# Performance work log

Hardware: AMD Instinct MI355X
Metric: run time of the kernel (lower is better)

Reference implementation:

```python
import jax, jax.numpy as jnp
import numpy as np

EPS = 1e-4


def setup_inputs() -> dict:
    key = jax.random.key(0)
    k1, k2, k3 = jax.random.split(key, 3)
    B, C, H, W = 8, 3, 1024, 1024
    n_axis, n_knots = 8, 16
    raw = jax.random.uniform(k1, (B, C, H, W), dtype=jnp.float32)
    ys = jax.random.uniform(k2, (B, n_axis, n_knots), dtype=jnp.float32)
    A = jax.random.normal(k3, (B, C, n_axis), dtype=jnp.float32)
    return {"raw": raw, "ys": ys, "A": A}


def reference(raw, ys, A):
    # raw: [B,3,H,W], ys: [B,n_axis,K], A: [B,3,n_axis]
    B, C, H, W = raw.shape
    K = ys.shape[-1]
    pinv_A = jnp.linalg.pinv(A)                      # [B, n_axis, 3]
    mins = jnp.sum(A * (A < 0), axis=1)              # [B, n_axis]
    maxs = jnp.sum(A * (A > 0), axis=1)              # [B, n_axis]

    # project pixels onto axes: [B, n_axis, H, W]
    f = jnp.einsum('bchw,bca->bahw', raw, A)

    # knot x-positions (uniform per batch/axis): [B, n_axis, K+2]
    t = jnp.linspace(0.0, 1.0, K + 2, dtype=raw.dtype)[None, None]
    xs = t * (maxs + EPS - mins)[..., None] + mins[..., None]
    ys_full = jnp.concatenate([mins[..., None], ys, maxs[..., None]], axis=-1)  # [B,A,K+2]
    dx = xs[..., 1] - xs[..., 0]                     # [B, n_axis]
    slopes = jnp.diff(ys_full, axis=-1) / dx[..., None]  # [B, n_axis, K+1]

    # segment index per pixel (replaces masked loop): floor((f - xs0)/dx)
    idx = jnp.clip(jnp.floor((f - mins[..., None, None]) / dx[..., None, None]),
                   0, K).astype(jnp.int32)           # [B, n_axis, H, W]

    idx_flat = idx.reshape(B, -1, H * W)             # [B, n_axis, HW]
    ys_hi = jnp.take_along_axis(ys_full, idx_flat + 1, axis=-1).reshape(f.shape)
    xs_hi = jnp.take_along_axis(xs, idx_flat + 1, axis=-1).reshape(f.shape)
    sl = jnp.take_along_axis(slopes, idx_flat, axis=-1).reshape(f.shape)

    est = ys_hi - (xs_hi - f) * sl                   # [B, n_axis, H, W]

    # project back to RGB: [B, 3, H, W]
    out = jnp.einsum('bahw,bac->bchw', est, pinv_A)
    return out
```

## Files before the change

kernel.cpp:

```cpp
#include <hip/hip_runtime.h>

#define EPS 1e-4f
#define NAXIS 8
#define NKNOTS 16
#define NSEG 17
#define WS_STRIDE 384

typedef float fv4 __attribute__((ext_vector_type(4)));

__global__ void spline_prep(const float* __restrict__ ys,
                            const float* __restrict__ A,
                            float* __restrict__ ws) {
    const int b = blockIdx.x;
    const float* Ab  = A  + (size_t)b * 3 * NAXIS;
    const float* ysb = ys + (size_t)b * NAXIS * NKNOTS;
    float* w = ws + (size_t)b * WS_STRIDE;
    __shared__ double Ginv[9];
    const int tid = threadIdx.x;

    if (tid == 0) {
        double G[9];
        for (int i = 0; i < 3; ++i)
            for (int j = 0; j < 3; ++j) {
                double s = 0.0;
                for (int a = 0; a < NAXIS; ++a)
                    s += (double)Ab[i * NAXIS + a] * (double)Ab[j * NAXIS + a];
                G[i * 3 + j] = s;
            }
        const double g00 = G[0], g01 = G[1], g02 = G[2];
        const double g11 = G[4], g12 = G[5], g22 = G[8];
        const double det = g00 * (g11 * g22 - g12 * g12)
                         - g01 * (g01 * g22 - g12 * g02)
                         + g02 * (g01 * g12 - g11 * g02);
        const double inv = 1.0 / det;
        Ginv[0] = (g11 * g22 - g12 * g12) * inv;
        Ginv[1] = (g02 * g12 - g01 * g22) * inv;
        Ginv[2] = (g01 * g12 - g02 * g11) * inv;
        Ginv[3] = Ginv[1];
        Ginv[4] = (g00 * g22 - g02 * g02) * inv;
        Ginv[5] = (g02 * g01 - g00 * g12) * inv;
        Ginv[6] = Ginv[2];
        Ginv[7] = Ginv[5];
        Ginv[8] = (g00 * g11 - g01 * g01) * inv;
    }
    __syncthreads();

    if (tid < 24) {
        const int a = tid / 3, c = tid % 3;
        double s = 0.0;
        for (int i = 0; i < 3; ++i)
            s += (double)Ab[i * NAXIS + a] * Ginv[i * 3 + c];
        w[a * 3 + c] = (float)s;
        float mn = 0.f, mx = 0.f;
        for (int i = 0; i < 3; ++i) {
            const float v = Ab[i * NAXIS + a];
            mn += fminf(v, 0.f);
            mx += fmaxf(v, 0.f);
        }
        const float invdx = 17.0f / (mx + EPS - mn);
        w[24 + a * 3 + c] = Ab[c * NAXIS + a] * invdx;
    }
    if (tid < NAXIS) {
        const int a = tid;
        float mn = 0.f, mx = 0.f;
        for (int c = 0; c < 3; ++c) {
            const float v = Ab[c * NAXIS + a];
            mn += fminf(v, 0.f);
            mx += fmaxf(v, 0.f);
        }
        const float range = mx + EPS - mn;
        const float invdx = 17.0f / range;
        w[48 + a] = -mn * invdx;
        float yf[NKNOTS + 2];
        yf[0] = mn;
        for (int k = 0; k < NKNOTS; ++k) yf[k + 1] = ysb[a * NKNOTS + k];
        yf[NKNOTS + 1] = mx;
        for (int s = 0; s < NSEG; ++s) {
            const float dy = yf[s + 1] - yf[s];
            w[64 + (a * NSEG + s) * 2 + 0] = dy;
            w[64 + (a * NSEG + s) * 2 + 1] = yf[s + 1] - (float)(s + 1) * dy;
        }
    }
}

__device__ __forceinline__ float rfl(float x) {
    return __int_as_float(__builtin_amdgcn_readfirstlane(__float_as_int(x)));
}

__global__ __launch_bounds__(256) void spline_main(const float* __restrict__ raw,
                                                   const float* __restrict__ ws,
                                                   float* __restrict__ out,
                                                   int blocksPerBatch, int HW) {
    const int b    = blockIdx.x / blocksPerBatch;
    const int tile = blockIdx.x % blocksPerBatch;

    const float* w = ws + (size_t)b * WS_STRIDE;

    const size_t base = (size_t)b * 3 * HW + (size_t)tile * 1024 + threadIdx.x * 4;
    const fv4 r4 = __builtin_nontemporal_load((const fv4*)(raw + base));
    const fv4 g4 = __builtin_nontemporal_load((const fv4*)(raw + base + HW));
    const fv4 b4 = __builtin_nontemporal_load((const fv4*)(raw + base + 2 * (size_t)HW));

    float cc[56];
    #pragma unroll
    for (int i = 0; i < 14; ++i) {
        const fv4 t = *(const fv4*)(w + 4 * i);
        cc[4 * i + 0] = rfl(t.x);
        cc[4 * i + 1] = rfl(t.y);
        cc[4 * i + 2] = rfl(t.z);
        cc[4 * i + 3] = rfl(t.w);
    }
    const float* cP = cc;
    const float* cA = cc + 24;
    const float* cO = cc + 48;

    __shared__ float2 sseg[NAXIS * NSEG];
    {
        const float2* wseg = (const float2*)(w + 64);
        for (int i = threadIdx.x; i < NAXIS * NSEG; i += 256)
            sseg[i] = wseg[i];
    }
    __syncthreads();

    fv4 o0, o1, o2;

    #pragma unroll
    for (int p = 0; p < 4; ++p) {
        const float rc = r4[p], gc = g4[p], bc = b4[p];
        float a0 = 0.f, a1 = 0.f, a2 = 0.f;
        #pragma unroll
        for (int a = 0; a < NAXIS; ++a) {
            const float u = fmaf(rc, cA[a * 3 + 0],
                             fmaf(gc, cA[a * 3 + 1],
                             fmaf(bc, cA[a * 3 + 2], cO[a])));
            const int idx = (int)fminf(fmaxf(u, 0.f), 16.0f);
            const float2 ci = sseg[a * NSEG + idx];
            const float est = fmaf(ci.x, u, ci.y);
            a0 = fmaf(est, cP[a * 3 + 0], a0);
            a1 = fmaf(est, cP[a * 3 + 1], a1);
            a2 = fmaf(est, cP[a * 3 + 2], a2);
        }
        o0[p] = a0; o1[p] = a1; o2[p] = a2;
    }

    __builtin_nontemporal_store(o0, (fv4*)(out + base));
    __builtin_nontemporal_store(o1, (fv4*)(out + base + HW));
    __builtin_nontemporal_store(o2, (fv4*)(out + base + 2 * (size_t)HW));
}

extern "C" void kernel_launch(void* const* d_in, const int* in_sizes, int n_in,
                              void* d_out, int out_size, void* d_ws, size_t ws_size,
                              hipStream_t stream) {
    const float* raw = (const float*)d_in[0];
    const float* ys  = (const float*)d_in[1];
    const float* A   = (const float*)d_in[2];
    float* out = (float*)d_out;
    float* ws  = (float*)d_ws;

    const int B  = in_sizes[2] / (3 * NAXIS);
    const int HW = in_sizes[0] / (B * 3);
    const int blocksPerBatch = HW / 1024;

    spline_prep<<<B, 64, 0, stream>>>(ys, A, ws);
    spline_main<<<B * blocksPerBatch, 256, 0, stream>>>(raw, ws, out, blocksPerBatch, HW);
}
```

Before: 176.1 us.

## Stage 2048-pixel tiles through LDS with wave-contiguous global loads and stores

Each block now handles 2048 pixels instead of 1024. Every wave loads contiguous 1536-float chunks across the three planes into registers, writes them to LDS, computes from LDS, writes the results back to LDS, and then stores them to global memory in the same contiguous pattern. The goal is longer contiguous memory streams per wave and more loads in flight per thread. The cost is 24KB of LDS per block, two extra barriers, and LDS round trips, all of which can lower occupancy.

```diff
diff --git a/kernel.cpp b/kernel.cpp
--- a/kernel.cpp
+++ b/kernel.cpp
@@ -5,6 +5,8 @@
 #define NKNOTS 16
 #define NSEG 17
 #define WS_STRIDE 384
+#define TPX 2048
+#define PLW 2048
 
 typedef float fv4 __attribute__((ext_vector_type(4)));
 
@@ -90,16 +92,27 @@
 __global__ __launch_bounds__(256) void spline_main(const float* __restrict__ raw,
                                                    const float* __restrict__ ws,
                                                    float* __restrict__ out,
-                                                   int blocksPerBatch, int HW) {
-    const int b    = blockIdx.x / blocksPerBatch;
-    const int tile = blockIdx.x % blocksPerBatch;
+                                                   int tilesPerBatch, int HW) {
+    const int b    = blockIdx.x / tilesPerBatch;
+    const int tile = blockIdx.x % tilesPerBatch;
 
     const float* w = ws + (size_t)b * WS_STRIDE;
 
-    const size_t base = (size_t)b * 3 * HW + (size_t)tile * 1024 + threadIdx.x * 4;
-    const fv4 r4 = __builtin_nontemporal_load((const fv4*)(raw + base));
-    const fv4 g4 = __builtin_nontemporal_load((const fv4*)(raw + base + HW));
-    const fv4 b4 = __builtin_nontemporal_load((const fv4*)(raw + base + 2 * (size_t)HW));
+    __shared__ float lds_t[3 * PLW];
+    __shared__ float2 sseg[NAXIS * NSEG];
+
+    const int wv = threadIdx.x >> 6;
+    const int ln = threadIdx.x & 63;
+    const size_t pbase = (size_t)b * 3 * HW + (size_t)tile * TPX;
+
+    fv4 stg[6];
+    #pragma unroll
+    for (int L = 0; L < 6; ++L) {
+        const int flat  = wv * 1536 + L * 256 + ln * 4;
+        const int plane = flat >> 11;
+        const int off   = flat & (PLW - 1);
+        stg[L] = __builtin_nontemporal_load((const fv4*)(raw + pbase + (size_t)plane * HW + off));
+    }
 
     float cc[56];
     #pragma unroll
@@ -114,38 +127,59 @@
     const float* cA = cc + 24;
     const float* cO = cc + 48;
 
-    __shared__ float2 sseg[NAXIS * NSEG];
     {
         const float2* wseg = (const float2*)(w + 64);
         for (int i = threadIdx.x; i < NAXIS * NSEG; i += 256)
             sseg[i] = wseg[i];
     }
+
+    #pragma unroll
+    for (int L = 0; L < 6; ++L) {
+        const int flat = wv * 1536 + L * 256 + ln * 4;
+        *(fv4*)(lds_t + flat) = stg[L];
+    }
     __syncthreads();
 
-    fv4 o0, o1, o2;
-
-    #pragma unroll
-    for (int p = 0; p < 4; ++p) {
-        const float rc = r4[p], gc = g4[p], bc = b4[p];
-        float a0 = 0.f, a1 = 0.f, a2 = 0.f;
+    const int t4 = threadIdx.x * 4;
+    #pragma unroll
+    for (int h = 0; h < 2; ++h) {
+        const int p0 = h * 1024 + t4;
+        const fv4 rr = *(const fv4*)(lds_t + p0);
+        const fv4 gg = *(const fv4*)(lds_t + PLW + p0);
+        const fv4 bb = *(const fv4*)(lds_t + 2 * PLW + p0);
+        fv4 o0, o1, o2;
         #pragma unroll
-        for (int a = 0; a < NAXIS; ++a) {
-            const float u = fmaf(rc, cA[a * 3 + 0],
-                             fmaf(gc, cA[a * 3 + 1],
-                             fmaf(bc, cA[a * 3 + 2], cO[a])));
-            const int idx = (int)fminf(fmaxf(u, 0.f), 16.0f);
-            const float2 ci = sseg[a * NSEG + idx];
-            const float est = fmaf(ci.x, u, ci.y);
-            a0 = fmaf(est, cP[a * 3 + 0], a0);
-            a1 = fmaf(est, cP[a * 3 + 1], a1);
-            a2 = fmaf(est, cP[a * 3 + 2], a2);
-        }
-        o0[p] = a0; o1[p] = a1; o2[p] = a2;
-    }
-
-    __builtin_nontemporal_store(o0, (fv4*)(out + base));
-    __builtin_nontemporal_store(o1, (fv4*)(out + base + HW));
-    __builtin_nontemporal_store(o2, (fv4*)(out + base + 2 * (size_t)HW));
+        for (int p = 0; p < 4; ++p) {
+            const float rc = rr[p], gc = gg[p], bc = bb[p];
+            float a0 = 0.f, a1 = 0.f, a2 = 0.f;
+            #pragma unroll
+            for (int a = 0; a < NAXIS; ++a) {
+                const float u = fmaf(rc, cA[a * 3 + 0],
+                                 fmaf(gc, cA[a * 3 + 1],
+                                 fmaf(bc, cA[a * 3 + 2], cO[a])));
+                const int idx = (int)fminf(fmaxf(u, 0.f), 16.0f);
+                const float2 ci = sseg[a * NSEG + idx];
+                const float est = fmaf(ci.x, u, ci.y);
+                a0 = fmaf(est, cP[a * 3 + 0], a0);
+                a1 = fmaf(est, cP[a * 3 + 1], a1);
+                a2 = fmaf(est, cP[a * 3 + 2], a2);
+            }
+            o0[p] = a0; o1[p] = a1; o2[p] = a2;
+        }
+        *(fv4*)(lds_t + p0)           = o0;
+        *(fv4*)(lds_t + PLW + p0)     = o1;
+        *(fv4*)(lds_t + 2 * PLW + p0) = o2;
+    }
+    __syncthreads();
+
+    #pragma unroll
+    for (int L = 0; L < 6; ++L) {
+        const int flat  = wv * 1536 + L * 256 + ln * 4;
+        const int plane = flat >> 11;
+        const int off   = flat & (PLW - 1);
+        const fv4 v = *(const fv4*)(lds_t + flat);
+        __builtin_nontemporal_store(v, (fv4*)(out + pbase + (size_t)plane * HW + off));
+    }
 }
 
 extern "C" void kernel_launch(void* const* d_in, const int* in_sizes, int n_in,
@@ -159,8 +193,8 @@
 
     const int B  = in_sizes[2] / (3 * NAXIS);
     const int HW = in_sizes[0] / (B * 3);
-    const int blocksPerBatch = HW / 1024;
+    const int tilesPerBatch = HW / TPX;
 
     spline_prep<<<B, 64, 0, stream>>>(ys, A, ws);
-    spline_main<<<B * blocksPerBatch, 256, 0, stream>>>(raw, ws, out, blocksPerBatch, HW);
-}
+    spline_main<<<B * tilesPerBatch, 256, 0, stream>>>(raw, ws, out, tilesPerBatch, HW);
+}
```

New measurement: 179.0 us. Within noise of the previous version (+1.6%).
